# Optimization experiments

Hardware: AMD Instinct MI355X
Metric: run time of the kernel (lower is better)

The kernel has to match this reference:

```python
import jax, jax.numpy as jnp
import numpy as np

N_NODES = 1_000_000
N_EDGES = 16_000_000
D = 30            # num_feature hardcoded in the module
WINDOW = D // 6   # = 5
DEG_THRESH = 10
NUM_TYPES = 2


def setup_inputs() -> dict:
    key = jax.random.key(0)
    k1, k2, k3, k4 = jax.random.split(key, 4)
    x = jax.random.normal(k1, (N_NODES, D), dtype=jnp.float32)
    W = jax.random.normal(k2, (D, D), dtype=jnp.float32)
    edge_index = jax.random.randint(k3, (2, N_EDGES), 0, N_NODES, dtype=jnp.int64)
    atom_types = jax.random.randint(k4, (N_NODES,), 0, NUM_TYPES, dtype=jnp.int64)
    return {"x": x, "W": W, "edge_index": edge_index, "atom_types": atom_types}


def reference(x, W, edge_index, atom_types):
    n = x.shape[0]
    # --- degree count: torch.bincount(edge_index.reshape(-1)) ---
    flat = edge_index.reshape(-1)
    count = jnp.zeros((n,), jnp.int32).at[flat].add(1)
    crit_count = (count > DEG_THRESH).astype(jnp.int32)  # criterion_count

    # --- type-mixture scatter-min over edges ---
    src, dst = edge_index[0], edge_index[1]
    same = atom_types[src] == atom_types[dst]
    # edge contributes 0 if types differ, else type+1, to BOTH endpoints; take min
    val = jnp.where(same, atom_types[src].astype(jnp.int32) + 1, 0)
    BIG = jnp.iinfo(jnp.int32).max
    mix = jnp.full((n,), BIG, jnp.int32)
    mix = mix.at[src].min(val).at[dst].min(val)
    mix = jnp.where(mix == BIG, 0, mix)  # isolated atoms -> 0

    crit = crit_count * 3 + mix  # criterion in [0, 5]

    # --- windowed one-hot criterion matrix [n, D] ---
    cols = jnp.arange(D, dtype=jnp.int32)
    start = (crit * WINDOW)[:, None]
    mask = ((cols[None, :] >= start) & (cols[None, :] < start + WINDOW)).astype(x.dtype)

    # --- e3nn Linear (30x0e -> 30x0e): dense matmul with 1/sqrt(fan_in) path norm ---
    scale = np.float32(1.0 / np.sqrt(D))
    return (x @ W) * scale * mask
```

## Files before the change

### kernel.cpp

```cpp
#include <hip/hip_runtime.h>

#define N_NODES    1000000
#define N_EDGES    16000000
#define D          30
#define WINDOW     5
#define DEG_THRESH 10

#define P_PARTS    31
#define PART_BITS  15
#define PART_SIZE  32768
#define CAP        1081344
#define BUF_CAP    512
#define BIN_BLOCKS 256
#define BIN_THREADS 1024
#define BIN_ITERS  16
#define N_GROUPS   (N_EDGES / 4)
#define BM_WORDS   (N_NODES / 32)

#define L_BM_BYTES   125000
#define L_BUF_BYTES  (P_PARTS * BUF_CAP * 2)
#define L_CNT_OFF    (L_BM_BYTES + L_BUF_BYTES)
#define L_TOTAL      (L_CNT_OFF + P_PARTS * 4 * 3)

#define SLICES     8
#define HIST_WORDS 16384

#define WS_BM_OFF      0
#define WS_CUR_OFF     131072
#define WS_PART_OFF    131328
#define WS_NEEDED      (WS_PART_OFF + (size_t)P_PARTS * SLICES * HIST_WORDS * 4)
#define OUT_BYTES_NEEDED ((size_t)P_PARTS * CAP * 2)

__global__ __launch_bounds__(256) void pack_types(
    const int* __restrict__ types,
    unsigned*  __restrict__ bm,
    unsigned*  __restrict__ cursors)
{
    const int g = blockIdx.x * 256 + threadIdx.x;
    const int v = (g < N_NODES) ? types[g] : 0;
    const unsigned long long m = __ballot(v);
    if ((threadIdx.x & 31) == 0 && g < N_NODES)
        bm[g >> 5] = (unsigned)(m >> (threadIdx.x & 32));
    if (blockIdx.x == 0 && threadIdx.x < 64) cursors[threadIdx.x] = 0u;
}

__global__ __launch_bounds__(BIN_THREADS, 1) void bin_edges(
    const int*      __restrict__ edge_index,
    const unsigned* __restrict__ bm,
    unsigned short* __restrict__ buckets,
    unsigned*       __restrict__ cursors)
{
    extern __shared__ char smem[];
    unsigned* bm_lds = (unsigned*)smem;
    unsigned short (*buf)[BUF_CAP] =
        (unsigned short(*)[BUF_CAP])(smem + L_BM_BYTES);
    unsigned* cnt   = (unsigned*)(smem + L_CNT_OFF);
    unsigned* basev = cnt + P_PARTS;
    unsigned* ccnt  = basev + P_PARTS;

    const int tid = threadIdx.x;
    for (int i = tid; i < BM_WORDS; i += BIN_THREADS) bm_lds[i] = bm[i];
    if (tid < P_PARTS) cnt[tid] = 0u;
    __syncthreads();

    for (int it = 0; it < BIN_ITERS; ++it) {
        const int g = (blockIdx.x * BIN_ITERS + it) * BIN_THREADS + tid;
        if (g < N_GROUPS) {
            const int e0 = g * 4;
            const int4 s4 = *reinterpret_cast<const int4*>(edge_index + e0);
            const int4 d4 = *reinterpret_cast<const int4*>(edge_index + N_EDGES + e0);
            const int ss[4] = {s4.x, s4.y, s4.z, s4.w};
            const int dd[4] = {d4.x, d4.y, d4.z, d4.w};
#pragma unroll
            for (int k = 0; k < 4; ++k) {
                const int s = ss[k], d = dd[k];
                const unsigned ts = (bm_lds[(unsigned)s >> 5] >> (s & 31)) & 1u;
                const unsigned td = (bm_lds[(unsigned)d >> 5] >> (d & 31)) & 1u;
                {
                    const int b = s >> PART_BITS;
                    const unsigned short rec =
                        (unsigned short)(((s & (PART_SIZE - 1)) << 1) | td);
                    const unsigned pos = atomicAdd(&cnt[b], 1u);
                    if (pos < BUF_CAP) buf[b][pos] = rec;
                    else {
                        const unsigned gp = atomicAdd(&cursors[b], 1u);
                        if (gp < CAP) buckets[(size_t)b * CAP + gp] = rec;
                    }
                }
                {
                    const int b = d >> PART_BITS;
                    const unsigned short rec =
                        (unsigned short)(((d & (PART_SIZE - 1)) << 1) | ts);
                    const unsigned pos = atomicAdd(&cnt[b], 1u);
                    if (pos < BUF_CAP) buf[b][pos] = rec;
                    else {
                        const unsigned gp = atomicAdd(&cursors[b], 1u);
                        if (gp < CAP) buckets[(size_t)b * CAP + gp] = rec;
                    }
                }
            }
        }
        __syncthreads();
        if (tid < P_PARTS) {
            unsigned c = cnt[tid]; if (c > BUF_CAP) c = BUF_CAP;
            unsigned bse = 0u;
            if (c) {
                bse = atomicAdd(&cursors[tid], c);
                if (bse > CAP) bse = CAP;
                if (bse + c > CAP) c = CAP - bse;
            }
            ccnt[tid] = c; basev[tid] = bse; cnt[tid] = 0u;
        }
        __syncthreads();
        const int w = tid >> 6, lane = tid & 63;
#pragma unroll
        for (int j = 0; j < 2; ++j) {
            const int b = w * 2 + j;
            if (b < P_PARTS) {
                const unsigned c = ccnt[b];
                unsigned short* dst = buckets + (size_t)b * CAP + basev[b];
                for (unsigned e = lane; e < c; e += 64) dst[e] = buf[b][e];
            }
        }
        __syncthreads();
    }
}

__global__ __launch_bounds__(512) void hist_pass(
    const unsigned short* __restrict__ buckets,
    const unsigned*       __restrict__ cursors,
    unsigned*             __restrict__ partials)
{
    __shared__ unsigned hist[HIST_WORDS];
    const int p = blockIdx.x >> 3, s = blockIdx.x & 7;
    const int tid = threadIdx.x;
    for (int i = tid; i < HIST_WORDS; i += 512) hist[i] = 0u;
    __syncthreads();

    unsigned count = cursors[p]; if (count > CAP) count = CAP;
    const unsigned short* bk = buckets + (size_t)p * CAP;
    const unsigned n4 = (count + 3u) >> 2;
    for (unsigned j = (unsigned)(s * 512 + tid); j < n4; j += SLICES * 512) {
        const unsigned i0 = j * 4u;
        if (i0 + 4u <= count) {
            const ushort4 r4 = *reinterpret_cast<const ushort4*>(bk + i0);
            const unsigned short rr[4] = {r4.x, r4.y, r4.z, r4.w};
#pragma unroll
            for (int k = 0; k < 4; ++k) {
                const unsigned rec = rr[k];
                const unsigned local = rec >> 1, t = rec & 1u;
                atomicAdd(&hist[local >> 1], (1u << (8u * t)) << (16u * (local & 1u)));
            }
        } else {
            for (unsigned i = i0; i < count; ++i) {
                const unsigned rec = bk[i];
                const unsigned local = rec >> 1, t = rec & 1u;
                atomicAdd(&hist[local >> 1], (1u << (8u * t)) << (16u * (local & 1u)));
            }
        }
    }
    __syncthreads();
    unsigned* op = partials + (size_t)blockIdx.x * HIST_WORDS;
    for (int i = tid; i < HIST_WORDS; i += 512) op[i] = hist[i];
}

#define WT_STRIDE  36
#define OT_THREADS 256
#define OT_ROWPAD  33
__global__ __launch_bounds__(OT_THREADS) void out_pass(
    const float* __restrict__ x, const float* __restrict__ Wm,
    const unsigned* __restrict__ partials,
    const unsigned* __restrict__ bm,
    float* __restrict__ out)
{
    __shared__ float sWt[D * WT_STRIDE];
    __shared__ float stg[OT_THREADS / 64][64 * OT_ROWPAD];
    const int tid = threadIdx.x;
    for (int i = tid; i < D * D; i += OT_THREADS) {
        const int k = i / D, c = i - k * D;
        sWt[c * WT_STRIDE + k] = Wm[i];
    }

    const int wv = tid >> 6, lane = tid & 63;
    const long blockBase = (long)blockIdx.x * OT_THREADS;
    const long waveBase  = blockBase + (long)wv * 64;
    float* ws = stg[wv];
    const long f4base = (waveBase >> 1) * 15;
    const long f4lim  = (long)N_NODES * (D / 2) / 2;

    const float4* gx = reinterpret_cast<const float4*>(x);
#pragma unroll
    for (int it = 0; it < 8; ++it) {
        const int g = it * 64 + lane;
        if (g < 480) {
            float4 v = make_float4(0.0f, 0.0f, 0.0f, 0.0f);
            if (f4base + g < f4lim) v = gx[f4base + g];
            const int pair = g / 15, within = g - pair * 15;
            const int r0 = pair * 2, f0 = within * 4;
            const float vv[4] = {v.x, v.y, v.z, v.w};
#pragma unroll
            for (int e = 0; e < 4; ++e) {
                const int ff = f0 + e;
                const int r  = r0 + (ff >= D);
                const int c  = ff - ((ff >= D) ? D : 0);
                ws[r * OT_ROWPAD + c] = vv[e];
            }
        }
    }
    __syncthreads();

    const long n = blockBase + tid;
    int start = 0;
    if (n < N_NODES) {
        const unsigned Wd   = (unsigned)(n >> 1);
        const unsigned h    = (unsigned)n & 1u;
        const unsigned p    = Wd >> 14;
        const unsigned widx = Wd & 16383u;
        const unsigned* pp  = partials + (size_t)(p * SLICES) * HIST_WORDS + widx;
        unsigned sum = 0u;
#pragma unroll
        for (int s = 0; s < SLICES; ++s) sum += pp[(size_t)s * HIST_WORDS];
        const unsigned c0 = (sum >> (16u * h)) & 0xFFu;
        const unsigned c1 = (sum >> (16u * h + 8u)) & 0xFFu;
        const unsigned t  = (bm[n >> 5] >> ((unsigned)n & 31u)) & 1u;
        const unsigned cnt    = c0 + c1;
        const unsigned same_c = t ? c1 : c0;
        const unsigned diff_c = t ? c0 : c1;
        const int mix  = diff_c ? 0 : (same_c ? (int)t + 1 : 0);
        const int crit = (cnt > DEG_THRESH ? 3 : 0) + mix;
        start = crit * WINDOW;
    }

    float xr[D];
#pragma unroll
    for (int k = 0; k < D; ++k) xr[k] = ws[lane * OT_ROWPAD + k];

    float acc[WINDOW];
    const float* wc0 = &sWt[start * WT_STRIDE];
#pragma unroll
    for (int j = 0; j < WINDOW; ++j) {
        const float* wc = wc0 + j * WT_STRIDE;
        float a = 0.0f;
#pragma unroll
        for (int k = 0; k < D; ++k) a += xr[k] * wc[k];
        acc[j] = a * 0.18257418583505536f;
    }
    __syncthreads();

    float* wr = ws + lane * OT_ROWPAD;
#pragma unroll
    for (int k = 0; k < D; ++k) wr[k] = 0.0f;
#pragma unroll
    for (int j = 0; j < WINDOW; ++j) wr[start + j] = acc[j];
    __syncthreads();

    float4* gout = reinterpret_cast<float4*>(out);
#pragma unroll
    for (int it = 0; it < 8; ++it) {
        const int g = it * 64 + lane;
        if (g < 480 && f4base + g < f4lim) {
            const int pair = g / 15, within = g - pair * 15;
            const int r0 = pair * 2, f0 = within * 4;
            float vv[4];
#pragma unroll
            for (int e = 0; e < 4; ++e) {
                const int ff = f0 + e;
                const int r  = r0 + (ff >= D);
                const int c  = ff - ((ff >= D) ? D : 0);
                vv[e] = ws[r * OT_ROWPAD + c];
            }
            gout[f4base + g] = make_float4(vv[0], vv[1], vv[2], vv[3]);
        }
    }
}

#define SAME_INC (1u << 12)
#define DIFF_INC (1u << 22)

__global__ __launch_bounds__(256) void edge_pass_atomic(
    const int* __restrict__ edge_index, const int* __restrict__ atom_types,
    unsigned* __restrict__ agg)
{
    const int t  = blockIdx.x * blockDim.x + threadIdx.x;
    const int e0 = t * 4;
    if (e0 >= N_EDGES) return;
    const int4 s4 = *reinterpret_cast<const int4*>(edge_index + e0);
    const int4 d4 = *reinterpret_cast<const int4*>(edge_index + N_EDGES + e0);
    const int ss[4] = {s4.x, s4.y, s4.z, s4.w};
    const int dd[4] = {d4.x, d4.y, d4.z, d4.w};
#pragma unroll
    for (int k = 0; k < 4; ++k) {
        const int s = ss[k], d = dd[k];
        const unsigned add = 1u + ((atom_types[s] == atom_types[d]) ? SAME_INC : DIFF_INC);
        atomicAdd(agg + s, add);
        atomicAdd(agg + d, add);
    }
}

__global__ __launch_bounds__(256) void out_pass_agg(
    const float* __restrict__ x, const float* __restrict__ Wm,
    const unsigned* __restrict__ agg, const int* __restrict__ atom_types,
    float* __restrict__ out)
{
    __shared__ float sx[64 * D];
    __shared__ float sW[D * D];
    __shared__ int   sstart[64];
    const int tid   = threadIdx.x;
    const long base = (long)blockIdx.x * 64;
    for (int i = tid; i < D * D; i += 256) sW[i] = Wm[i];
    const float* xb = x + base * D;
    for (int i = tid; i < 64 * D; i += 256) sx[i] = xb[i];
    if (tid < 64) {
        const long n = base + tid;
        const unsigned a = agg[n];
        const int cnt = a & 0xFFFu, sc = (a >> 12) & 0x3FFu, dc = a >> 22;
        const int mix  = dc ? 0 : (sc ? atom_types[n] + 1 : 0);
        sstart[tid] = ((cnt > DEG_THRESH ? 3 : 0) + mix) * WINDOW;
    }
    __syncthreads();
    const float scale = 0.18257418583505536f;
    float* ob = out + base * D;
    for (int i = tid; i < 64 * D; i += 256) {
        const int nd = i / D, c = i - nd * D;
        float v = 0.0f;
        if ((unsigned)(c - sstart[nd]) < WINDOW) {
            float acc = 0.0f;
#pragma unroll
            for (int k = 0; k < D; ++k) acc += sx[nd * D + k] * sW[k * D + c];
            v = acc * scale;
        }
        ob[i] = v;
    }
}

extern "C" void kernel_launch(void* const* d_in, const int* in_sizes, int n_in,
                              void* d_out, int out_size, void* d_ws, size_t ws_size,
                              hipStream_t stream)
{
    const float* x          = (const float*)d_in[0];
    const float* Wm         = (const float*)d_in[1];
    const int*   edge_index = (const int*)d_in[2];
    const int*   atom_types = (const int*)d_in[3];
    float* out = (float*)d_out;

    if (ws_size >= WS_NEEDED && (size_t)out_size * 4 >= OUT_BYTES_NEEDED) {
        char* ws = (char*)d_ws;
        unsigned*       bm       = (unsigned*)(ws + WS_BM_OFF);
        unsigned*       cursors  = (unsigned*)(ws + WS_CUR_OFF);
        unsigned*       partials = (unsigned*)(ws + WS_PART_OFF);
        unsigned short* buckets  = (unsigned short*)d_out;

        pack_types<<<(N_NODES + 255) / 256, 256, 0, stream>>>(atom_types, bm, cursors);
        bin_edges<<<BIN_BLOCKS, BIN_THREADS, L_TOTAL, stream>>>(edge_index, bm,
                                                                buckets, cursors);
        hist_pass<<<P_PARTS * SLICES, 512, 0, stream>>>(buckets, cursors, partials);
        out_pass<<<(N_NODES + OT_THREADS - 1) / OT_THREADS, OT_THREADS, 0, stream>>>(
            x, Wm, partials, bm, out);
    } else {
        unsigned* agg = (unsigned*)d_ws;
        hipMemsetAsync(agg, 0x00, N_NODES * sizeof(unsigned), stream);
        edge_pass_atomic<<<(N_EDGES / 4) / 256, 256, 0, stream>>>(edge_index, atom_types, agg);
        out_pass_agg<<<N_NODES / 64, 256, 0, stream>>>(x, Wm, agg, atom_types, out);
    }
}
```

Measured before the change: 374.7 us.

## Replace global bucket cursors with per-block private cells in edge binning

Each binning block now writes into its own fixed-size slot per partition, tracked by an LDS cursor, so the global atomicAdd on shared partition cursors is no longer needed. Per-cell counts are stored and the histogram pass iterates over the cells of its slice. This removes contention on global atomics, but the histogram reads become fragmented across many small cells and each cell has a fixed capacity, which could drop edges if a block overflows it.

```diff
diff --git a/kernel.cpp b/kernel.cpp
--- a/kernel.cpp
+++ b/kernel.cpp
@@ -9,7 +9,6 @@
 #define P_PARTS    31
 #define PART_BITS  15
 #define PART_SIZE  32768
-#define CAP        1081344
 #define BUF_CAP    512
 #define BIN_BLOCKS 256
 #define BIN_THREADS 1024
@@ -17,38 +16,42 @@
 #define N_GROUPS   (N_EDGES / 4)
 #define BM_WORDS   (N_NODES / 32)
 
+#define NCELL      BIN_BLOCKS
+#define SLOT_CAP   6400
+#define BK_BYTES   ((size_t)P_PARTS * NCELL * SLOT_CAP * 2)
+#define CCNT_OFF   BK_BYTES
+#define OUT_BYTES_NEEDED (BK_BYTES + (size_t)P_PARTS * NCELL * 4)
+
 #define L_BM_BYTES   125000
 #define L_BUF_BYTES  (P_PARTS * BUF_CAP * 2)
 #define L_CNT_OFF    (L_BM_BYTES + L_BUF_BYTES)
-#define L_TOTAL      (L_CNT_OFF + P_PARTS * 4 * 3)
+#define L_TOTAL      (L_CNT_OFF + P_PARTS * 4 * 4)
 
 #define SLICES     8
+#define CELLS_PER_SLICE (NCELL / SLICES)
 #define HIST_WORDS 16384
 
 #define WS_BM_OFF      0
 #define WS_CUR_OFF     131072
 #define WS_PART_OFF    131328
 #define WS_NEEDED      (WS_PART_OFF + (size_t)P_PARTS * SLICES * HIST_WORDS * 4)
-#define OUT_BYTES_NEEDED ((size_t)P_PARTS * CAP * 2)
 
 __global__ __launch_bounds__(256) void pack_types(
     const int* __restrict__ types,
-    unsigned*  __restrict__ bm,
-    unsigned*  __restrict__ cursors)
+    unsigned*  __restrict__ bm)
 {
     const int g = blockIdx.x * 256 + threadIdx.x;
     const int v = (g < N_NODES) ? types[g] : 0;
     const unsigned long long m = __ballot(v);
     if ((threadIdx.x & 31) == 0 && g < N_NODES)
         bm[g >> 5] = (unsigned)(m >> (threadIdx.x & 32));
-    if (blockIdx.x == 0 && threadIdx.x < 64) cursors[threadIdx.x] = 0u;
 }
 
 __global__ __launch_bounds__(BIN_THREADS, 1) void bin_edges(
     const int*      __restrict__ edge_index,
     const unsigned* __restrict__ bm,
     unsigned short* __restrict__ buckets,
-    unsigned*       __restrict__ cursors)
+    unsigned*       __restrict__ cellcnt)
 {
     extern __shared__ char smem[];
     unsigned* bm_lds = (unsigned*)smem;
@@ -57,11 +60,14 @@
     unsigned* cnt   = (unsigned*)(smem + L_CNT_OFF);
     unsigned* basev = cnt + P_PARTS;
     unsigned* ccnt  = basev + P_PARTS;
+    unsigned* ccur  = ccnt + P_PARTS;
 
     const int tid = threadIdx.x;
     for (int i = tid; i < BM_WORDS; i += BIN_THREADS) bm_lds[i] = bm[i];
-    if (tid < P_PARTS) cnt[tid] = 0u;
-    __syncthreads();
+    if (tid < P_PARTS) { cnt[tid] = 0u; ccur[tid] = 0u; }
+    __syncthreads();
+
+    const size_t cellbase0 = (size_t)blockIdx.x * SLOT_CAP;
 
     for (int it = 0; it < BIN_ITERS; ++it) {
         const int g = (blockIdx.x * BIN_ITERS + it) * BIN_THREADS + tid;
@@ -83,8 +89,9 @@
                     const unsigned pos = atomicAdd(&cnt[b], 1u);
                     if (pos < BUF_CAP) buf[b][pos] = rec;
                     else {
-                        const unsigned gp = atomicAdd(&cursors[b], 1u);
-                        if (gp < CAP) buckets[(size_t)b * CAP + gp] = rec;
+                        const unsigned gp = atomicAdd(&ccur[b], 1u);
+                        if (gp < SLOT_CAP)
+                            buckets[(size_t)b * NCELL * SLOT_CAP + cellbase0 + gp] = rec;
                     }
                 }
                 {
@@ -94,8 +101,9 @@
                     const unsigned pos = atomicAdd(&cnt[b], 1u);
                     if (pos < BUF_CAP) buf[b][pos] = rec;
                     else {
-                        const unsigned gp = atomicAdd(&cursors[b], 1u);
-                        if (gp < CAP) buckets[(size_t)b * CAP + gp] = rec;
+                        const unsigned gp = atomicAdd(&ccur[b], 1u);
+                        if (gp < SLOT_CAP)
+                            buckets[(size_t)b * NCELL * SLOT_CAP + cellbase0 + gp] = rec;
                     }
                 }
             }
@@ -103,12 +111,10 @@
         __syncthreads();
         if (tid < P_PARTS) {
             unsigned c = cnt[tid]; if (c > BUF_CAP) c = BUF_CAP;
-            unsigned bse = 0u;
-            if (c) {
-                bse = atomicAdd(&cursors[tid], c);
-                if (bse > CAP) bse = CAP;
-                if (bse + c > CAP) c = CAP - bse;
-            }
+            unsigned bse = ccur[tid];
+            if (bse > SLOT_CAP) bse = SLOT_CAP;
+            if (bse + c > SLOT_CAP) c = SLOT_CAP - bse;
+            ccur[tid] = bse + c;
             ccnt[tid] = c; basev[tid] = bse; cnt[tid] = 0u;
         }
         __syncthreads();
@@ -118,17 +124,23 @@
             const int b = w * 2 + j;
             if (b < P_PARTS) {
                 const unsigned c = ccnt[b];
-                unsigned short* dst = buckets + (size_t)b * CAP + basev[b];
+                unsigned short* dst =
+                    buckets + (size_t)b * NCELL * SLOT_CAP + cellbase0 + basev[b];
                 for (unsigned e = lane; e < c; e += 64) dst[e] = buf[b][e];
             }
         }
         __syncthreads();
+    }
+
+    if (tid < P_PARTS) {
+        unsigned c = ccur[tid]; if (c > SLOT_CAP) c = SLOT_CAP;
+        cellcnt[tid * NCELL + blockIdx.x] = c;
     }
 }
 
 __global__ __launch_bounds__(512) void hist_pass(
     const unsigned short* __restrict__ buckets,
-    const unsigned*       __restrict__ cursors,
+    const unsigned*       __restrict__ cellcnt,
     unsigned*             __restrict__ partials)
 {
     __shared__ unsigned hist[HIST_WORDS];
@@ -137,13 +149,14 @@
     for (int i = tid; i < HIST_WORDS; i += 512) hist[i] = 0u;
     __syncthreads();
 
-    unsigned count = cursors[p]; if (count > CAP) count = CAP;
-    const unsigned short* bk = buckets + (size_t)p * CAP;
-    const unsigned n4 = (count + 3u) >> 2;
-    for (unsigned j = (unsigned)(s * 512 + tid); j < n4; j += SLICES * 512) {
-        const unsigned i0 = j * 4u;
-        if (i0 + 4u <= count) {
-            const ushort4 r4 = *reinterpret_cast<const ushort4*>(bk + i0);
+    for (int cell = s * CELLS_PER_SLICE; cell < (s + 1) * CELLS_PER_SLICE; ++cell) {
+        unsigned count = cellcnt[p * NCELL + cell];
+        if (count > SLOT_CAP) count = SLOT_CAP;
+        const unsigned short* bk =
+            buckets + ((size_t)p * NCELL + cell) * SLOT_CAP;
+        const unsigned n4 = count >> 2;
+        for (unsigned j = (unsigned)tid; j < n4; j += 512) {
+            const ushort4 r4 = *reinterpret_cast<const ushort4*>(bk + j * 4u);
             const unsigned short rr[4] = {r4.x, r4.y, r4.z, r4.w};
 #pragma unroll
             for (int k = 0; k < 4; ++k) {
@@ -151,12 +164,11 @@
                 const unsigned local = rec >> 1, t = rec & 1u;
                 atomicAdd(&hist[local >> 1], (1u << (8u * t)) << (16u * (local & 1u)));
             }
-        } else {
-            for (unsigned i = i0; i < count; ++i) {
-                const unsigned rec = bk[i];
-                const unsigned local = rec >> 1, t = rec & 1u;
-                atomicAdd(&hist[local >> 1], (1u << (8u * t)) << (16u * (local & 1u)));
-            }
+        }
+        for (unsigned i = (n4 << 2) + (unsigned)tid; i < count; i += 512) {
+            const unsigned rec = bk[i];
+            const unsigned local = rec >> 1, t = rec & 1u;
+            atomicAdd(&hist[local >> 1], (1u << (8u * t)) << (16u * (local & 1u)));
         }
     }
     __syncthreads();
@@ -346,14 +358,14 @@
     if (ws_size >= WS_NEEDED && (size_t)out_size * 4 >= OUT_BYTES_NEEDED) {
         char* ws = (char*)d_ws;
         unsigned*       bm       = (unsigned*)(ws + WS_BM_OFF);
-        unsigned*       cursors  = (unsigned*)(ws + WS_CUR_OFF);
         unsigned*       partials = (unsigned*)(ws + WS_PART_OFF);
         unsigned short* buckets  = (unsigned short*)d_out;
-
-        pack_types<<<(N_NODES + 255) / 256, 256, 0, stream>>>(atom_types, bm, cursors);
+        unsigned*       cellcnt  = (unsigned*)((char*)d_out + CCNT_OFF);
+
+        pack_types<<<(N_NODES + 255) / 256, 256, 0, stream>>>(atom_types, bm);
         bin_edges<<<BIN_BLOCKS, BIN_THREADS, L_TOTAL, stream>>>(edge_index, bm,
-                                                                buckets, cursors);
-        hist_pass<<<P_PARTS * SLICES, 512, 0, stream>>>(buckets, cursors, partials);
+                                                                buckets, cellcnt);
+        hist_pass<<<P_PARTS * SLICES, 512, 0, stream>>>(buckets, cellcnt, partials);
         out_pass<<<(N_NODES + OT_THREADS - 1) / OT_THREADS, OT_THREADS, 0, stream>>>(
             x, Wm, partials, bm, out);
     } else {
```

Result: slower. 383.2 us (+2.3%).
